# Optimization experiments

Measured on AMD Instinct MI355X. Metric: run time of the kernel, lower is better.

The kernel has to match this reference:

```python
import math
import jax, jax.numpy as jnp
import numpy as np

B, L, D, H = 4, 2048, 1024, 16
HS = D // H  # 64


def setup_inputs() -> dict:
    key = jax.random.key(0)
    ks = jax.random.split(key, 6)
    x = jax.random.normal(ks[0], (B, L, D), dtype=jnp.float32)
    W_attn = jax.random.normal(ks[1], (D, 3 * D), dtype=jnp.float32) * 0.02
    b_attn = jnp.zeros((3 * D,), dtype=jnp.float32)
    W_proj = jax.random.normal(ks[2], (D, D), dtype=jnp.float32) * 0.02
    b_proj = jnp.zeros((D,), dtype=jnp.float32)
    Er = jax.random.normal(ks[3], (L, HS), dtype=jnp.float32)  # block_size == L
    return {"x": x, "W_attn": W_attn, "b_attn": b_attn,
            "W_proj": W_proj, "b_proj": b_proj, "Er": Er}


def _skew(QEr):
    # QEr: [B, H, L, L] -> pad one column on the left, reshape, drop first row.
    b, h, r, c = QEr.shape
    padded = jnp.pad(QEr, ((0, 0), (0, 0), (0, 0), (1, 0)))  # [B,H,L,L+1]
    return padded.reshape(b, h, c + 1, r)[:, :, 1:, :]        # [B,H,L,L]


def reference(x, W_attn, b_attn, W_proj, b_proj, Er):
    b, l, d = x.shape
    qkv = x @ W_attn + b_attn                     # [B,L,3D]
    q, k, v = jnp.split(qkv, 3, axis=2)
    q = q.reshape(b, l, H, HS).transpose(0, 2, 1, 3)  # [B,H,L,hs]
    k = k.reshape(b, l, H, HS).transpose(0, 2, 1, 3)
    v = v.reshape(b, l, H, HS).transpose(0, 2, 1, 3)
    # start = block_size - L = 0 here; Er_t: [hs, L]
    Er_t = Er[Er.shape[0] - l:, :].T
    QEr = jnp.einsum('bhld,dm->bhlm', q, Er_t)    # [B,H,L,L]
    Srel = _skew(QEr)
    scale = 1.0 / math.sqrt(HS)
    att = (jnp.einsum('bhqd,bhkd->bhqk', q, k) + Srel) * scale
    causal = jnp.tril(jnp.ones((l, l), dtype=bool))
    att = jnp.where(causal[None, None, :, :], att, -jnp.inf)
    att = jax.nn.softmax(att, axis=-1)
    y = jnp.einsum('bhqk,bhkd->bhqd', att, v)     # [B,H,L,hs]
    y = y.transpose(0, 2, 1, 3).reshape(b, l, d)
    return y @ W_proj + b_proj
```

## Files before the change

kernel.cpp:

```cpp
#include <hip/hip_runtime.h>
#include <hip/hip_bf16.h>
#include <math.h>

#define B_  4
#define L_  2048
#define D_  1024
#define H_  16
#define HS_ 64
#define SCALE 0.125f

typedef unsigned short ushort_t;
typedef __attribute__((ext_vector_type(8))) short short8;
typedef __attribute__((ext_vector_type(4))) float f32x4;

static __device__ __forceinline__ ushort_t f2bf(float f) {
    union { float f; unsigned int u; } cv; cv.f = f;
    unsigned int u = cv.u;
    unsigned int r = (u + 0x7FFFu + ((u >> 16) & 1u)) >> 16;
    return (ushort_t)r;
}

static __device__ __forceinline__ void gload_lds16(const ushort_t* g, ushort_t* l) {
    __builtin_amdgcn_global_load_lds(
        (const __attribute__((address_space(1))) unsigned int*)g,
        (__attribute__((address_space(3))) unsigned int*)l, 16, 0, 0);
}

__global__ __launch_bounds__(256)
void conv_to_bf16(const float* __restrict__ x, ushort_t* __restrict__ xb)
{
    const size_t i = (size_t)blockIdx.x * 256 + threadIdx.x;
    const float4* src = (const float4*)x + i * 2;
    float4 a = src[0], b = src[1];
    ushort_t o[8] = {f2bf(a.x), f2bf(a.y), f2bf(a.z), f2bf(a.w),
                     f2bf(b.x), f2bf(b.y), f2bf(b.z), f2bf(b.w)};
    *(uint4*)(xb + i * 8) = *(uint4*)o;
}

__global__ __launch_bounds__(256)
void transpose_to_bf16(const float* __restrict__ W, ushort_t* __restrict__ Wt,
                       int K, int N)
{
    __shared__ ushort_t tile[64][65];
    const int tid = threadIdx.x;
    const int n0 = blockIdx.x * 64, k0 = blockIdx.y * 64;
#pragma unroll
    for (int s = 0; s < 16; ++s) {
        const int idx = s * 256 + tid;
        const int kl = idx >> 6, nl = idx & 63;
        tile[nl][kl] = f2bf(W[(size_t)(k0 + kl) * N + n0 + nl]);
    }
    __syncthreads();
#pragma unroll
    for (int s = 0; s < 8; ++s) {
        const int idx = s * 256 + tid;
        const int nl = idx >> 5, kc = idx & 31;
        const unsigned int vlo = tile[nl][kc * 2];
        const unsigned int vhi = tile[nl][kc * 2 + 1];
        *(unsigned int*)(Wt + (size_t)(n0 + nl) * K + k0 + kc * 2) =
            vlo | (vhi << 16);
    }
}

__global__ __launch_bounds__(256)
void qkv_mfma(const ushort_t* __restrict__ A, const ushort_t* __restrict__ Bt,
              const float* __restrict__ bias, ushort_t* __restrict__ qkv)
{
    __shared__ __align__(16) ushort_t As[128 * 64];
    __shared__ __align__(16) ushort_t Bs[128 * 64];

    const int tid = threadIdx.x;
    const int w = tid >> 6, lane = tid & 63, quad = lane >> 4, lcol = lane & 15;
    const int wr = w >> 1, wc = w & 1;
    const int m0 = blockIdx.y * 128, n0 = blockIdx.x * 128;
    const int K = D_;

    const int srow = tid >> 3;
    const int cg = (tid & 7) ^ (srow & 7);
    const ushort_t* gA = A + (size_t)(m0 + srow) * K + cg * 8;
    const ushort_t* gB = Bt + (size_t)(n0 + srow) * K + cg * 8;
    ushort_t* lA = As + tid * 8;
    ushort_t* lB = Bs + tid * 8;

    const int cs0 = ((quad) ^ (lcol & 7)) * 8;
    const int cs1 = ((4 + quad) ^ (lcol & 7)) * 8;

    f32x4 acc[4][4];
#pragma unroll
    for (int i = 0; i < 4; ++i)
#pragma unroll
        for (int j = 0; j < 4; ++j) acc[i][j] = (f32x4){0, 0, 0, 0};

    for (int k0 = 0; k0 < K; k0 += 64) {
        __syncthreads();
#pragma unroll
        for (int s = 0; s < 4; ++s) {
            gload_lds16(gA + k0 + (size_t)s * 32 * K, lA + s * 2048);
            gload_lds16(gB + k0 + (size_t)s * 32 * K, lB + s * 2048);
        }
        __syncthreads();
#pragma unroll
        for (int kk = 0; kk < 2; ++kk) {
            const int cs = kk ? cs1 : cs0;
            short8 af[4], bf[4];
#pragma unroll
            for (int i = 0; i < 4; ++i)
                af[i] = *(const short8*)&As[(wr * 64 + i * 16 + lcol) * 64 + cs];
#pragma unroll
            for (int j = 0; j < 4; ++j)
                bf[j] = *(const short8*)&Bs[(wc * 64 + j * 16 + lcol) * 64 + cs];
#pragma unroll
            for (int i = 0; i < 4; ++i)
#pragma unroll
                for (int j = 0; j < 4; ++j)
                    acc[i][j] = __builtin_amdgcn_mfma_f32_16x16x32_bf16(
                        af[i], bf[j], acc[i][j], 0, 0, 0);
        }
    }

    const size_t per = (size_t)B_ * H_ * L_ * HS_;
#pragma unroll
    for (int j = 0; j < 4; ++j) {
        const int col = n0 + wc * 64 + j * 16 + lcol;
        const float bv = bias[col];
        const int sel = col >> 10;
        const int within = col & 1023;
        const int hh = within >> 6, hs = within & 63;
        if (sel < 2) {
            ushort_t* base = qkv + (size_t)sel * per;
#pragma unroll
            for (int i = 0; i < 4; ++i) {
#pragma unroll
                for (int reg = 0; reg < 4; ++reg) {
                    const int row = m0 + wr * 64 + i * 16 + quad * 4 + reg;
                    const int bb = row >> 11, ll = row & 2047;
                    base[(((size_t)(bb * H_ + hh)) * L_ + ll) * HS_ + hs] =
                        f2bf(acc[i][j][reg] + bv);
                }
            }
        } else {
            ushort_t* base = qkv + 2 * per;
#pragma unroll
            for (int i = 0; i < 4; ++i) {
#pragma unroll
                for (int reg = 0; reg < 4; ++reg) {
                    const int row = m0 + wr * 64 + i * 16 + quad * 4 + reg;
                    const int bb = row >> 11, ll = row & 2047;
                    base[(((size_t)(bb * H_ + hh)) * HS_ + hs) * L_ + ll] =
                        f2bf(acc[i][j][reg] + bv);
                }
            }
        }
    }
}

__global__ __launch_bounds__(256)
void proj_mfma(const ushort_t* __restrict__ A, const ushort_t* __restrict__ Bt,
               const float* __restrict__ bias, float* __restrict__ C)
{
    __shared__ __align__(16) ushort_t As[128 * 64];
    __shared__ __align__(16) ushort_t Bs[128 * 64];

    const int tid = threadIdx.x;
    const int w = tid >> 6, lane = tid & 63, quad = lane >> 4, lcol = lane & 15;
    const int wr = w >> 1, wc = w & 1;
    const int m0 = blockIdx.y * 128, n0 = blockIdx.x * 128;
    const int K = D_;
    const int N = D_;

    const int srow = tid >> 3;
    const int cg = (tid & 7) ^ (srow & 7);
    const ushort_t* gA = A + (size_t)(m0 + srow) * K + cg * 8;
    const ushort_t* gB = Bt + (size_t)(n0 + srow) * K + cg * 8;
    ushort_t* lA = As + tid * 8;
    ushort_t* lB = Bs + tid * 8;

    const int cs0 = ((quad) ^ (lcol & 7)) * 8;
    const int cs1 = ((4 + quad) ^ (lcol & 7)) * 8;

    f32x4 acc[4][4];
#pragma unroll
    for (int i = 0; i < 4; ++i)
#pragma unroll
        for (int j = 0; j < 4; ++j) acc[i][j] = (f32x4){0, 0, 0, 0};

    for (int k0 = 0; k0 < K; k0 += 64) {
        __syncthreads();
#pragma unroll
        for (int s = 0; s < 4; ++s) {
            gload_lds16(gA + k0 + (size_t)s * 32 * K, lA + s * 2048);
            gload_lds16(gB + k0 + (size_t)s * 32 * K, lB + s * 2048);
        }
        __syncthreads();
#pragma unroll
        for (int kk = 0; kk < 2; ++kk) {
            const int cs = kk ? cs1 : cs0;
            short8 af[4], bf[4];
#pragma unroll
            for (int i = 0; i < 4; ++i)
                af[i] = *(const short8*)&As[(wr * 64 + i * 16 + lcol) * 64 + cs];
#pragma unroll
            for (int j = 0; j < 4; ++j)
                bf[j] = *(const short8*)&Bs[(wc * 64 + j * 16 + lcol) * 64 + cs];
#pragma unroll
            for (int i = 0; i < 4; ++i)
#pragma unroll
                for (int j = 0; j < 4; ++j)
                    acc[i][j] = __builtin_amdgcn_mfma_f32_16x16x32_bf16(
                        af[i], bf[j], acc[i][j], 0, 0, 0);
        }
    }

#pragma unroll
    for (int j = 0; j < 4; ++j) {
        const int col = n0 + wc * 64 + j * 16 + lcol;
        const float bv = bias[col];
#pragma unroll
        for (int i = 0; i < 4; ++i) {
#pragma unroll
            for (int reg = 0; reg < 4; ++reg) {
                const int row = m0 + wr * 64 + i * 16 + quad * 4 + reg;
                C[(size_t)row * N + col] = acc[i][j][reg] + bv;
            }
        }
    }
}

#define MFMA16(a, b, c) __builtin_amdgcn_mfma_f32_16x16x32_bf16(a, b, c, 0, 0, 0)

#define RING_STORE(C1) do {                                                       \
    if (w == 0)      { Ring[((C1)+5)&7]=e0; Ring[((C1)+6)&7]=e1;                  \
                       Ring[((C1)+7)&7]=e2; Ring[((C1)+8)&7]=e3; }                \
    else if (w == 1) { Ring[((C1)+6)&7]=e0; Ring[((C1)+7)&7]=e1;                  \
                       Ring[((C1)+8)&7]=e2; Ring[((C1)+9)&7]=e3; }                \
    else if (w == 2) { Ring[((C1)+7)&7]=e0; Ring[((C1)+8)&7]=e1;                  \
                       Ring[((C1)+9)&7]=e2; Ring[((C1)+10)&7]=e3; }               \
    else             { Ring[((C1)+8)&7]=e0; Ring[((C1)+9)&7]=e1;                  \
                       Ring[((C1)+10)&7]=e2; Ring[((C1)+11)&7]=e3; }              \
} while (0)

#define ATTN_ITER(KTv, C0, C1) {                                                  \
    const int kj0 = (KTv) * 64;                                                   \
    const bool diag = ((KTv) == qt);                                              \
    __syncthreads();                                                              \
    gload_lds16(kp + (size_t)(kj0 + srow) * 64 + cg8, Ks + tid * 8);              \
    gload_lds16(kp + (size_t)(kj0 + srow + 32) * 64 + cg8, Ks + tid * 8 + 2048);  \
    gload_lds16(vtp + (size_t)srow * L_ + kj0 + cg8, Vts + tid * 8);              \
    gload_lds16(vtp + (size_t)(srow + 32) * L_ + kj0 + cg8, Vts + tid * 8 + 2048);\
    { int m1 = cband + ((KTv) + 1) * 64 + srow; if (m1 > L_ - 1) m1 = L_ - 1;     \
      int m2 = cband + ((KTv) + 1) * 64 + srow + 32; if (m2 > L_ - 1) m2 = L_ - 1;\
      gload_lds16(er + (size_t)m1 * 64 + cg8, Es + tid * 8);                      \
      gload_lds16(er + (size_t)m2 * 64 + cg8, Es + tid * 8 + 2048); }             \
    __syncthreads();                                                              \
    f32x4 S0 = {0,0,0,0}, S1 = {0,0,0,0}, S2 = {0,0,0,0}, S3 = {0,0,0,0};         \
    f32x4 e0 = {0,0,0,0}, e1 = {0,0,0,0}, e2 = {0,0,0,0}, e3 = {0,0,0,0};         \
    S0 = MFMA16(aq0, *(const short8*)&Ks[( 0 + lcol) * 64 + fr0], S0);            \
    S1 = MFMA16(aq0, *(const short8*)&Ks[(16 + lcol) * 64 + fr0], S1);            \
    S2 = MFMA16(aq0, *(const short8*)&Ks[(32 + lcol) * 64 + fr0], S2);            \
    S3 = MFMA16(aq0, *(const short8*)&Ks[(48 + lcol) * 64 + fr0], S3);            \
    S0 = MFMA16(aq1, *(const short8*)&Ks[( 0 + lcol) * 64 + fr1], S0);            \
    S1 = MFMA16(aq1, *(const short8*)&Ks[(16 + lcol) * 64 + fr1], S1);            \
    S2 = MFMA16(aq1, *(const short8*)&Ks[(32 + lcol) * 64 + fr1], S2);            \
    S3 = MFMA16(aq1, *(const short8*)&Ks[(48 + lcol) * 64 + fr1], S3);            \
    e0 = MFMA16(aq0, *(const short8*)&Es[( 0 + lcol) * 64 + fr0], e0);            \
    e1 = MFMA16(aq0, *(const short8*)&Es[(16 + lcol) * 64 + fr0], e1);            \
    e2 = MFMA16(aq0, *(const short8*)&Es[(32 + lcol) * 64 + fr0], e2);            \
    e3 = MFMA16(aq0, *(const short8*)&Es[(48 + lcol) * 64 + fr0], e3);            \
    e0 = MFMA16(aq1, *(const short8*)&Es[( 0 + lcol) * 64 + fr1], e0);            \
    e1 = MFMA16(aq1, *(const short8*)&Es[(16 + lcol) * 64 + fr1], e1);            \
    e2 = MFMA16(aq1, *(const short8*)&Es[(32 + lcol) * 64 + fr1], e2);            \
    e3 = MFMA16(aq1, *(const short8*)&Es[(48 + lcol) * 64 + fr1], e3);            \
    RING_STORE(C1);                                                               \
    f32x4 S[4] = {S0, S1, S2, S3};                                                \
    _Pragma("unroll")                                                             \
    for (int reg = 0; reg < 4; ++reg) {                                           \
        const int qr = quad * 4 + reg;                                            \
        const int srcl = quad * 16 + ((15 - qr + lcol) & 15);                     \
        const bool carry = (lcol > qr);                                           \
        float psum = 0.f;                                                         \
        _Pragma("unroll")                                                         \
        for (int nt = 0; nt < 4; ++nt) {                                          \
            const float v0 = __shfl(Ring[((C0) + nt) & 7][reg], srcl, 64);        \
            const float v1 = __shfl(Ring[((C0) + nt + 1) & 7][reg], srcl, 64);    \
            const float ev = carry ? v1 : v0;                                     \
            const float sv = (S[nt][reg] + ev) * SCALE;                           \
            float p = __expf(sv);                                                 \
            if (diag && (nt * 16 + lcol > w * 16 + qr)) p = 0.f;                  \
            psum += p;                                                            \
            Ps[(w * 16 + qr) * 64 +                                               \
               (((nt * 2 + (lcol >> 3)) ^ (qr & 7)) * 8) + (lcol & 7)] = f2bf(p); \
        }                                                                         \
        psum += __shfl_xor(psum, 1);                                              \
        psum += __shfl_xor(psum, 2);                                              \
        psum += __shfl_xor(psum, 4);                                              \
        psum += __shfl_xor(psum, 8);                                              \
        l_r[reg] += psum;                                                         \
    }                                                                             \
    const short8 ap0 = *(const short8*)&Ps[(w * 16 + lcol) * 64 + fr0];           \
    const short8 ap1 = *(const short8*)&Ps[(w * 16 + lcol) * 64 + fr1];           \
    O[0] = MFMA16(ap0, *(const short8*)&Vts[( 0 + lcol) * 64 + fr0], O[0]);       \
    O[1] = MFMA16(ap0, *(const short8*)&Vts[(16 + lcol) * 64 + fr0], O[1]);       \
    O[2] = MFMA16(ap0, *(const short8*)&Vts[(32 + lcol) * 64 + fr0], O[2]);       \
    O[3] = MFMA16(ap0, *(const short8*)&Vts[(48 + lcol) * 64 + fr0], O[3]);       \
    O[0] = MFMA16(ap1, *(const short8*)&Vts[( 0 + lcol) * 64 + fr1], O[0]);       \
    O[1] = MFMA16(ap1, *(const short8*)&Vts[(16 + lcol) * 64 + fr1], O[1]);       \
    O[2] = MFMA16(ap1, *(const short8*)&Vts[(32 + lcol) * 64 + fr1], O[2]);       \
    O[3] = MFMA16(ap1, *(const short8*)&Vts[(48 + lcol) * 64 + fr1], O[3]);       \
}

__global__ __launch_bounds__(256, 4)
void attn_mfma(const ushort_t* __restrict__ q, const ushort_t* __restrict__ k,
               const ushort_t* __restrict__ vt, const ushort_t* __restrict__ er,
               ushort_t* __restrict__ y)
{
    __shared__ __align__(16) ushort_t Qs[64 * 64];
    __shared__ __align__(16) ushort_t Ks[64 * 64];
    __shared__ __align__(16) ushort_t Vts[64 * 64];
    __shared__ __align__(16) ushort_t Es[64 * 64];
    __shared__ __align__(16) ushort_t Ps[64 * 64];

    const int tid  = threadIdx.x;
    const int w    = tid >> 6;
    const int lane = tid & 63;
    const int quad = lane >> 4;
    const int lcol = lane & 15;

    const int n  = blockIdx.x;
    const int cc = n & 7;
    const int mm = n >> 3;
    const int bh = cc + 8 * (mm >> 5);
    const int qt = 31 - (mm & 31);

    const int qi0  = qt * 64;
    const int bb   = bh >> 4;
    const int hh   = bh & 15;
    const int cband = L_ - 64 - qi0;

    const ushort_t* qp  = q + (size_t)bh * L_ * HS_;
    const ushort_t* kp  = k + (size_t)bh * L_ * HS_;
    const ushort_t* vtp = vt + (size_t)bh * HS_ * L_;

    const int srow = tid >> 3;
    const int cg8  = ((tid & 7) ^ (srow & 7)) * 8;

    gload_lds16(qp + (size_t)(qi0 + srow) * 64 + cg8, Qs + tid * 8);
    gload_lds16(qp + (size_t)(qi0 + srow + 32) * 64 + cg8, Qs + tid * 8 + 2048);
    gload_lds16(er + (size_t)(cband + srow) * 64 + cg8, Es + tid * 8);
    gload_lds16(er + (size_t)(cband + srow + 32) * 64 + cg8, Es + tid * 8 + 2048);
    __syncthreads();

    const int fr0 = ((quad) ^ (lcol & 7)) * 8;
    const int fr1 = ((4 + quad) ^ (lcol & 7)) * 8;
    const short8 aq0 = *(const short8*)&Qs[(w * 16 + lcol) * 64 + fr0];
    const short8 aq1 = *(const short8*)&Qs[(w * 16 + lcol) * 64 + fr1];

    f32x4 Ring[8];
    {
        f32x4 e0 = {0,0,0,0}, e1 = {0,0,0,0}, e2 = {0,0,0,0}, e3 = {0,0,0,0};
        e0 = MFMA16(aq0, *(const short8*)&Es[( 0 + lcol) * 64 + fr0], e0);
        e1 = MFMA16(aq0, *(const short8*)&Es[(16 + lcol) * 64 + fr0], e1);
        e2 = MFMA16(aq0, *(const short8*)&Es[(32 + lcol) * 64 + fr0], e2);
        e3 = MFMA16(aq0, *(const short8*)&Es[(48 + lcol) * 64 + fr0], e3);
        e0 = MFMA16(aq1, *(const short8*)&Es[( 0 + lcol) * 64 + fr1], e0);
        e1 = MFMA16(aq1, *(const short8*)&Es[(16 + lcol) * 64 + fr1], e1);
        e2 = MFMA16(aq1, *(const short8*)&Es[(32 + lcol) * 64 + fr1], e2);
        e3 = MFMA16(aq1, *(const short8*)&Es[(48 + lcol) * 64 + fr1], e3);
        RING_STORE(0);
    }

    f32x4 O[4];
#pragma unroll
    for (int nt = 0; nt < 4; ++nt) O[nt] = (f32x4){0, 0, 0, 0};
    float l_r[4] = {0, 0, 0, 0};

    for (int kt = 0; kt <= qt; kt += 2) {
        ATTN_ITER(kt, 0, 4);
        if (kt + 1 <= qt) ATTN_ITER(kt + 1, 4, 0);
    }

    float inv[4];
#pragma unroll
    for (int reg = 0; reg < 4; ++reg) inv[reg] = 1.f / l_r[reg];
#pragma unroll
    for (int nt = 0; nt < 4; ++nt) {
#pragma unroll
        for (int reg = 0; reg < 4; ++reg) {
            const int r = w * 16 + quad * 4 + reg;
            Ps[r * 64 + nt * 16 + lcol] = f2bf(O[nt][reg] * inv[reg]);
        }
    }
    __syncthreads();
#pragma unroll
    for (int s = 0; s < 2; ++s) {
        const int idx = tid + s * 256;
        const int row = idx >> 3;
        const int c8  = (idx & 7) * 8;
        *(uint4*)(y + (((size_t)bb * L_ + qi0 + row) * H_ + hh) * HS_ + c8) =
            *(const uint4*)&Ps[row * 64 + c8];
    }
}

extern "C" void kernel_launch(void* const* d_in, const int* in_sizes, int n_in,
                              void* d_out, int out_size, void* d_ws, size_t ws_size,
                              hipStream_t stream)
{
    const float* x      = (const float*)d_in[0];
    const float* W_attn = (const float*)d_in[1];
    const float* b_attn = (const float*)d_in[2];
    const float* W_proj = (const float*)d_in[3];
    const float* b_proj = (const float*)d_in[4];
    const float* Er     = (const float*)d_in[5];
    float* out = (float*)d_out;

    const size_t per = (size_t)B_ * H_ * L_ * HS_;
    ushort_t* qb  = (ushort_t*)d_ws;
    ushort_t* kb  = qb + per;
    ushort_t* vtb = kb + per;
    ushort_t* yb  = vtb + per;
    ushort_t* xb  = yb + per;
    ushort_t* wat = xb + per;
    ushort_t* wpt = wat + (size_t)3 * D_ * D_;
    ushort_t* erb = wpt + (size_t)D_ * D_;

    dim3 blk(256);

    conv_to_bf16<<<dim3((B_ * L_ * D_) / 2048), blk, 0, stream>>>(x, xb);
    conv_to_bf16<<<dim3((L_ * HS_) / 2048), blk, 0, stream>>>(Er, erb);
    transpose_to_bf16<<<dim3(3 * D_ / 64, D_ / 64), blk, 0, stream>>>(W_attn, wat, D_, 3 * D_);
    transpose_to_bf16<<<dim3(D_ / 64, D_ / 64), blk, 0, stream>>>(W_proj, wpt, D_, D_);

    qkv_mfma<<<dim3(3 * D_ / 128, B_ * L_ / 128), blk, 0, stream>>>(xb, wat, b_attn, qb);

    attn_mfma<<<dim3((L_ / 64) * B_ * H_), blk, 0, stream>>>(qb, kb, vtb, erb, yb);

    proj_mfma<<<dim3(D_ / 128, B_ * L_ / 128), blk, 0, stream>>>(yb, wpt, b_proj, out);
}
```

Measured before the change: 635.5 us.

## Pair complementary causal query tiles per block to balance attention work

Each attention block now processes two query tiles, 31-p and p, so every block covers the same total number of causal key tiles. The grid halves from 2048 to 1024 blocks. The second phase walks key tiles in reverse, so the Er prologue and ring-buffer bookkeeping are generalised with a new-column parameter. This removes the tail imbalance of the triangular workload, but each block now runs longer and there are fewer blocks in total.

```diff
diff --git a/kernel.cpp b/kernel.cpp
--- a/kernel.cpp
+++ b/kernel.cpp
@@ -239,7 +239,7 @@
                        Ring[((C1)+10)&7]=e2; Ring[((C1)+11)&7]=e3; }              \
 } while (0)
 
-#define ATTN_ITER(KTv, C0, C1) {                                                  \
+#define ATTN_ITER(KTv, C0v, SBv, CNEWv) {                                         \
     const int kj0 = (KTv) * 64;                                                   \
     const bool diag = ((KTv) == qt);                                              \
     __syncthreads();                                                              \
@@ -247,8 +247,8 @@
     gload_lds16(kp + (size_t)(kj0 + srow + 32) * 64 + cg8, Ks + tid * 8 + 2048);  \
     gload_lds16(vtp + (size_t)srow * L_ + kj0 + cg8, Vts + tid * 8);              \
     gload_lds16(vtp + (size_t)(srow + 32) * L_ + kj0 + cg8, Vts + tid * 8 + 2048);\
-    { int m1 = cband + ((KTv) + 1) * 64 + srow; if (m1 > L_ - 1) m1 = L_ - 1;     \
-      int m2 = cband + ((KTv) + 1) * 64 + srow + 32; if (m2 > L_ - 1) m2 = L_ - 1;\
+    { int m1 = cband + (CNEWv) * 64 + srow; if (m1 > L_ - 1) m1 = L_ - 1;         \
+      int m2 = cband + (CNEWv) * 64 + srow + 32; if (m2 > L_ - 1) m2 = L_ - 1;    \
       gload_lds16(er + (size_t)m1 * 64 + cg8, Es + tid * 8);                      \
       gload_lds16(er + (size_t)m2 * 64 + cg8, Es + tid * 8 + 2048); }             \
     __syncthreads();                                                              \
@@ -270,7 +270,7 @@
     e1 = MFMA16(aq1, *(const short8*)&Es[(16 + lcol) * 64 + fr1], e1);            \
     e2 = MFMA16(aq1, *(const short8*)&Es[(32 + lcol) * 64 + fr1], e2);            \
     e3 = MFMA16(aq1, *(const short8*)&Es[(48 + lcol) * 64 + fr1], e3);            \
-    RING_STORE(C1);                                                               \
+    RING_STORE(SBv);                                                              \
     f32x4 S[4] = {S0, S1, S2, S3};                                                \
     _Pragma("unroll")                                                             \
     for (int reg = 0; reg < 4; ++reg) {                                           \
@@ -280,8 +280,8 @@
         float psum = 0.f;                                                         \
         _Pragma("unroll")                                                         \
         for (int nt = 0; nt < 4; ++nt) {                                          \
-            const float v0 = __shfl(Ring[((C0) + nt) & 7][reg], srcl, 64);        \
-            const float v1 = __shfl(Ring[((C0) + nt + 1) & 7][reg], srcl, 64);    \
+            const float v0 = __shfl(Ring[((C0v) + nt) & 7][reg], srcl, 64);       \
+            const float v1 = __shfl(Ring[((C0v) + nt + 1) & 7][reg], srcl, 64);   \
             const float ev = carry ? v1 : v0;                                     \
             const float sv = (S[nt][reg] + ev) * SCALE;                           \
             float p = __expf(sv);                                                 \
@@ -325,16 +325,11 @@
     const int quad = lane >> 4;
     const int lcol = lane & 15;
 
-    const int n  = blockIdx.x;
-    const int cc = n & 7;
-    const int mm = n >> 3;
-    const int bh = cc + 8 * (mm >> 5);
-    const int qt = 31 - (mm & 31);
-
-    const int qi0  = qt * 64;
+    const int n    = blockIdx.x;
+    const int bh   = (n & 7) + 8 * (n >> 7);
+    const int pidx = (n >> 3) & 15;
     const int bb   = bh >> 4;
     const int hh   = bh & 15;
-    const int cband = L_ - 64 - qi0;
 
     const ushort_t* qp  = q + (size_t)bh * L_ * HS_;
     const ushort_t* kp  = k + (size_t)bh * L_ * HS_;
@@ -342,61 +337,84 @@
 
     const int srow = tid >> 3;
     const int cg8  = ((tid & 7) ^ (srow & 7)) * 8;
-
-    gload_lds16(qp + (size_t)(qi0 + srow) * 64 + cg8, Qs + tid * 8);
-    gload_lds16(qp + (size_t)(qi0 + srow + 32) * 64 + cg8, Qs + tid * 8 + 2048);
-    gload_lds16(er + (size_t)(cband + srow) * 64 + cg8, Es + tid * 8);
-    gload_lds16(er + (size_t)(cband + srow + 32) * 64 + cg8, Es + tid * 8 + 2048);
-    __syncthreads();
-
     const int fr0 = ((quad) ^ (lcol & 7)) * 8;
     const int fr1 = ((4 + quad) ^ (lcol & 7)) * 8;
-    const short8 aq0 = *(const short8*)&Qs[(w * 16 + lcol) * 64 + fr0];
-    const short8 aq1 = *(const short8*)&Qs[(w * 16 + lcol) * 64 + fr1];
 
     f32x4 Ring[8];
-    {
-        f32x4 e0 = {0,0,0,0}, e1 = {0,0,0,0}, e2 = {0,0,0,0}, e3 = {0,0,0,0};
-        e0 = MFMA16(aq0, *(const short8*)&Es[( 0 + lcol) * 64 + fr0], e0);
-        e1 = MFMA16(aq0, *(const short8*)&Es[(16 + lcol) * 64 + fr0], e1);
-        e2 = MFMA16(aq0, *(const short8*)&Es[(32 + lcol) * 64 + fr0], e2);
-        e3 = MFMA16(aq0, *(const short8*)&Es[(48 + lcol) * 64 + fr0], e3);
-        e0 = MFMA16(aq1, *(const short8*)&Es[( 0 + lcol) * 64 + fr1], e0);
-        e1 = MFMA16(aq1, *(const short8*)&Es[(16 + lcol) * 64 + fr1], e1);
-        e2 = MFMA16(aq1, *(const short8*)&Es[(32 + lcol) * 64 + fr1], e2);
-        e3 = MFMA16(aq1, *(const short8*)&Es[(48 + lcol) * 64 + fr1], e3);
-        RING_STORE(0);
-    }
-
-    f32x4 O[4];
-#pragma unroll
-    for (int nt = 0; nt < 4; ++nt) O[nt] = (f32x4){0, 0, 0, 0};
-    float l_r[4] = {0, 0, 0, 0};
-
-    for (int kt = 0; kt <= qt; kt += 2) {
-        ATTN_ITER(kt, 0, 4);
-        if (kt + 1 <= qt) ATTN_ITER(kt + 1, 4, 0);
-    }
-
-    float inv[4];
-#pragma unroll
-    for (int reg = 0; reg < 4; ++reg) inv[reg] = 1.f / l_r[reg];
-#pragma unroll
-    for (int nt = 0; nt < 4; ++nt) {
-#pragma unroll
-        for (int reg = 0; reg < 4; ++reg) {
-            const int r = w * 16 + quad * 4 + reg;
-            Ps[r * 64 + nt * 16 + lcol] = f2bf(O[nt][reg] * inv[reg]);
-        }
-    }
-    __syncthreads();
-#pragma unroll
-    for (int s = 0; s < 2; ++s) {
-        const int idx = tid + s * 256;
-        const int row = idx >> 3;
-        const int c8  = (idx & 7) * 8;
-        *(uint4*)(y + (((size_t)bb * L_ + qi0 + row) * H_ + hh) * HS_ + c8) =
-            *(const uint4*)&Ps[row * 64 + c8];
+
+#pragma unroll
+    for (int ph = 0; ph < 2; ++ph) {
+        const int qt    = ph ? pidx : 31 - pidx;
+        const int qi0   = qt * 64;
+        const int cband = L_ - 64 - qi0;
+        const int cpro  = ph ? (qt + 1) : 0;
+
+        __syncthreads();
+        gload_lds16(qp + (size_t)(qi0 + srow) * 64 + cg8, Qs + tid * 8);
+        gload_lds16(qp + (size_t)(qi0 + srow + 32) * 64 + cg8, Qs + tid * 8 + 2048);
+        {
+            int m1 = cband + cpro * 64 + srow;      if (m1 > L_ - 1) m1 = L_ - 1;
+            int m2 = cband + cpro * 64 + srow + 32; if (m2 > L_ - 1) m2 = L_ - 1;
+            gload_lds16(er + (size_t)m1 * 64 + cg8, Es + tid * 8);
+            gload_lds16(er + (size_t)m2 * 64 + cg8, Es + tid * 8 + 2048);
+        }
+        __syncthreads();
+
+        const short8 aq0 = *(const short8*)&Qs[(w * 16 + lcol) * 64 + fr0];
+        const short8 aq1 = *(const short8*)&Qs[(w * 16 + lcol) * 64 + fr1];
+
+        {
+            f32x4 e0 = {0,0,0,0}, e1 = {0,0,0,0}, e2 = {0,0,0,0}, e3 = {0,0,0,0};
+            e0 = MFMA16(aq0, *(const short8*)&Es[( 0 + lcol) * 64 + fr0], e0);
+            e1 = MFMA16(aq0, *(const short8*)&Es[(16 + lcol) * 64 + fr0], e1);
+            e2 = MFMA16(aq0, *(const short8*)&Es[(32 + lcol) * 64 + fr0], e2);
+            e3 = MFMA16(aq0, *(const short8*)&Es[(48 + lcol) * 64 + fr0], e3);
+            e0 = MFMA16(aq1, *(const short8*)&Es[( 0 + lcol) * 64 + fr1], e0);
+            e1 = MFMA16(aq1, *(const short8*)&Es[(16 + lcol) * 64 + fr1], e1);
+            e2 = MFMA16(aq1, *(const short8*)&Es[(32 + lcol) * 64 + fr1], e2);
+            e3 = MFMA16(aq1, *(const short8*)&Es[(48 + lcol) * 64 + fr1], e3);
+            if (cpro & 1) { RING_STORE(4); } else { RING_STORE(0); }
+        }
+
+        f32x4 O[4];
+#pragma unroll
+        for (int nt = 0; nt < 4; ++nt) O[nt] = (f32x4){0, 0, 0, 0};
+        float l_r[4] = {0, 0, 0, 0};
+
+        if (ph == 0) {
+            for (int kt = 0; kt <= qt; kt += 2) {
+                ATTN_ITER(kt, 0, 4, kt + 1);
+                if (kt + 1 <= qt) ATTN_ITER(kt + 1, 4, 0, kt + 2);
+            }
+        } else {
+            int kt = qt;
+            if (kt & 1) { ATTN_ITER(kt, 4, 4, kt); --kt; }
+            for (; kt >= 0; kt -= 2) {
+                ATTN_ITER(kt, 0, 0, kt);
+                if (kt >= 1) ATTN_ITER(kt - 1, 4, 4, kt - 1);
+            }
+        }
+
+        float inv[4];
+#pragma unroll
+        for (int reg = 0; reg < 4; ++reg) inv[reg] = 1.f / l_r[reg];
+#pragma unroll
+        for (int nt = 0; nt < 4; ++nt) {
+#pragma unroll
+            for (int reg = 0; reg < 4; ++reg) {
+                const int r = w * 16 + quad * 4 + reg;
+                Ps[r * 64 + nt * 16 + lcol] = f2bf(O[nt][reg] * inv[reg]);
+            }
+        }
+        __syncthreads();
+#pragma unroll
+        for (int s = 0; s < 2; ++s) {
+            const int idx = tid + s * 256;
+            const int row = idx >> 3;
+            const int c8  = (idx & 7) * 8;
+            *(uint4*)(y + (((size_t)bb * L_ + qi0 + row) * H_ + hh) * HS_ + c8) =
+                *(const uint4*)&Ps[row * 64 + c8];
+        }
     }
 }
 
@@ -431,7 +449,7 @@
 
     qkv_mfma<<<dim3(3 * D_ / 128, B_ * L_ / 128), blk, 0, stream>>>(xb, wat, b_attn, qb);
 
-    attn_mfma<<<dim3((L_ / 64) * B_ * H_), blk, 0, stream>>>(qb, kb, vtb, erb, yb);
+    attn_mfma<<<dim3(1024), blk, 0, stream>>>(qb, kb, vtb, erb, yb);
 
     proj_mfma<<<dim3(D_ / 128, B_ * L_ / 128), blk, 0, stream>>>(yb, wpt, b_proj, out);
 }
```

Result: faster. 595.1 us (-6.4%).
